# Optimization experiments

Measured on AMD Instinct MI355X. Metric: run time of the kernel, lower is better.

## Reference

```python
import jax, jax.numpy as jnp
import numpy as np

B, S, D = 4, 2048, 1024

def setup_inputs() -> dict:
    key = jax.random.key(0)
    k0, k1, k2, k3 = jax.random.split(key, 4)
    scale = 1.0 / np.sqrt(D)
    return {
        "x": jax.random.normal(k0, (B, S, D), dtype=jnp.float32),
        "Wq": jax.random.normal(k1, (D, D), dtype=jnp.float32) * scale,
        "Wk": jax.random.normal(k2, (D, D), dtype=jnp.float32) * scale,
        "Wv": jax.random.normal(k3, (D, D), dtype=jnp.float32) * scale,
    }

def reference(x, Wq, Wk, Wv):
    # x: [B,S,D]; Wq/Wk/Wv: [D_in, D_out] (equivalent to torch Linear weight transposed)
    q = jnp.einsum('bsd,de->bse', x, Wq)
    k = jnp.einsum('bsd,de->bse', x, Wk)
    v = jnp.einsum('bsd,de->bse', x, Wv)
    d_out = k.shape[-1]
    scores = jnp.einsum('bqe,bke->bqk', q, k)  # [B,S,S]
    S_ = scores.shape[-1]
    causal = jnp.tril(jnp.ones((S_, S_), dtype=bool))  # True = keep
    # masked_fill before scaling == after scaling (-inf invariant under positive scale)
    scores = jnp.where(causal, scores, -jnp.inf)
    attn = jax.nn.softmax(scores / jnp.sqrt(jnp.asarray(d_out, scores.dtype)), axis=-1)
    # dropout p=0.0 -> identity
    return jnp.einsum('bqk,bke->bqe', attn, v)
```

## Files before the change

### kernel.cpp

```cpp
#include <hip/hip_runtime.h>

#define B_  4
#define S_  2048
#define D_  1024
#define N_  (B_*S_)
#define SCALE 0.03125f
#define NEGINF (-3.0e38f)

typedef unsigned short u16;
typedef __attribute__((ext_vector_type(8))) short short8;
typedef __attribute__((ext_vector_type(4))) float floatx4;

__device__ __forceinline__ u16 f2bf(float f) {
    unsigned int u = __float_as_uint(f);
    u += 0x7FFFu + ((u >> 16) & 1u);
    return (u16)(u >> 16);
}
__device__ __forceinline__ float bf2f(u16 h) {
    return __uint_as_float((unsigned int)h << 16);
}

__device__ __forceinline__ void gl_lds16(const void* g, void* l) {
    __builtin_amdgcn_global_load_lds(
        (const __attribute__((address_space(1))) unsigned int*)g,
        (__attribute__((address_space(3))) unsigned int*)l, 16, 0, 0);
}

__device__ __forceinline__ int xcd_chunk(int bid, int nwg) {
    return (bid & 7) * (nwg >> 3) + (bid >> 3);
}

__global__ __launch_bounds__(256) void cast_fused(const float* __restrict__ x,
                                                  const float* __restrict__ Wq, const float* __restrict__ Wk,
                                                  const float* __restrict__ Wv,
                                                  u16* __restrict__ xb, u16* __restrict__ Wqb,
                                                  u16* __restrict__ Wkb, u16* __restrict__ Wvt) {
    __shared__ float t[32][33];
    const int blk = blockIdx.x;
    if (blk < 5120) {
        const float* src; u16* dst; size_t i;
        if (blk < 4096)      { src = x;  dst = xb;  i = (size_t)blk * 2048; }
        else if (blk < 4608) { src = Wq; dst = Wqb; i = (size_t)(blk - 4096) * 2048; }
        else                 { src = Wk; dst = Wkb; i = (size_t)(blk - 4608) * 2048; }
        i += (size_t)threadIdx.x * 8;
        float4 a = *(const float4*)&src[i];
        float4 b = *(const float4*)&src[i + 4];
        short8 o;
        o[0]=f2bf(a.x); o[1]=f2bf(a.y); o[2]=f2bf(a.z); o[3]=f2bf(a.w);
        o[4]=f2bf(b.x); o[5]=f2bf(b.y); o[6]=f2bf(b.z); o[7]=f2bf(b.w);
        *(short8*)&dst[i] = o;
    } else {
        const int tb = blk - 5120;
        const int c = threadIdx.x & 31, r0 = threadIdx.x >> 5;
        const int i0 = (tb >> 5) * 32, j0 = (tb & 31) * 32;
#pragma unroll
        for (int rr = 0; rr < 4; ++rr)
            t[r0 + rr * 8][c] = Wv[(size_t)(i0 + r0 + rr * 8) * D_ + j0 + c];
        __syncthreads();
#pragma unroll
        for (int rr = 0; rr < 4; ++rr)
            Wvt[(size_t)(j0 + r0 + rr * 8) * D_ + i0 + c] = f2bf(t[c][r0 + rr * 8]);
    }
}


__device__ __forceinline__ void mfma_nt_128(const u16* __restrict__ A, int lda,
                                            const u16* __restrict__ Bp, int ldb,
                                            int m0, int n0, int kext,
                                            u16* Sh, floatx4 acc[4][4])
{
    const int tid  = threadIdx.x;
    const int lane = tid & 63;
    const int lr   = lane & 15, quad = lane >> 4;
    const int wm   = ((tid >> 6) & 1) * 64, wn = (tid >> 7) * 64;
    const int nt   = kext >> 6;

    auto stage8 = [&](int t) {
#pragma unroll
        for (int h = 0; h < 8; ++h) {
            const int kk = h >> 2, mat = (h >> 1) & 1, half = h & 1;
            const int idx = tid * 8;
            const int row = half * 64 + (idx >> 5);
            const int s   = (idx & 31) >> 3;
            const int gk  = (t << 6) + kk * 32 + ((s ^ ((row >> 1) & 3)) << 3);
            u16* dst = Sh + (t & 1) * 16384 + mat * 8192 + kk * 4096 + half * 2048 + idx;
            const u16* src = mat ? &Bp[(size_t)(n0 + row) * ldb + gk]
                                 : &A [(size_t)(m0 + row) * lda + gk];
            gl_lds16(src, dst);
        }
    };

    stage8(0);
    for (int t = 0; t < nt; ++t) {
        asm volatile("s_waitcnt vmcnt(0)" ::: "memory");
        __builtin_amdgcn_s_barrier();
        if (t + 1 < nt) stage8(t + 1);
        const u16* buf = Sh + (t & 1) * 16384;
#pragma unroll
        for (int kk = 0; kk < 2; ++kk) {
            short8 af[4], bf[4];
#pragma unroll
            for (int i = 0; i < 4; ++i) {
                const int ar = wm + i * 16 + lr;
                af[i] = *(const short8*)&buf[kk * 4096 + ar * 32 + ((quad ^ ((ar >> 1) & 3)) << 3)];
                const int br = wn + i * 16 + lr;
                bf[i] = *(const short8*)&buf[8192 + kk * 4096 + br * 32 + ((quad ^ ((br >> 1) & 3)) << 3)];
            }
            __builtin_amdgcn_s_setprio(1);
#pragma unroll
            for (int i = 0; i < 4; ++i)
#pragma unroll
                for (int j = 0; j < 4; ++j)
                    acc[i][j] = __builtin_amdgcn_mfma_f32_16x16x32_bf16(af[i], bf[j], acc[i][j], 0, 0, 0);
            __builtin_amdgcn_s_setprio(0);
        }
    }
}

#define EPI_VARS                                              \
    const int lane = threadIdx.x & 63;                        \
    const int lr = lane & 15, quad = lane >> 4;               \
    const int wm = ((threadIdx.x >> 6) & 1) * 64, wn = (threadIdx.x >> 7) * 64;

__device__ __forceinline__ void mfma_nt_128w8(const u16* __restrict__ A, int lda,
                                              const u16* __restrict__ Bp, int ldb,
                                              int m0, int n0, int kext,
                                              u16* Sh, floatx4 acc[2][4])
{
    const int tid  = threadIdx.x;
    const int lane = tid & 63;
    const int lr   = lane & 15, quad = lane >> 4;
    const int wid  = tid >> 6;
    const int wm   = (wid >> 1) * 32;
    const int wn   = (wid & 1) * 64;
    const int nt   = kext >> 6;

    auto stage4 = [&](int t) {
#pragma unroll
        for (int h = 0; h < 4; ++h) {
            const int kk = h >> 1, mat = h & 1;
            const int idx = tid * 8;
            const int row = idx >> 5;
            const int s   = (idx & 31) >> 3;
            const int gk  = (t << 6) + kk * 32 + ((s ^ ((row >> 1) & 3)) << 3);
            u16* dst = Sh + (t & 1) * 16384 + mat * 8192 + kk * 4096 + idx;
            const u16* src = mat ? &Bp[(size_t)(n0 + row) * ldb + gk]
                                 : &A [(size_t)(m0 + row) * lda + gk];
            gl_lds16(src, dst);
        }
    };

    stage4(0);
    for (int t = 0; t < nt; ++t) {
        asm volatile("s_waitcnt vmcnt(0)" ::: "memory");
        __builtin_amdgcn_s_barrier();
        if (t + 1 < nt) stage4(t + 1);
        const u16* buf = Sh + (t & 1) * 16384;
#pragma unroll
        for (int kk = 0; kk < 2; ++kk) {
            short8 af[2], bf[4];
#pragma unroll
            for (int i = 0; i < 2; ++i) {
                const int ar = wm + i * 16 + lr;
                af[i] = *(const short8*)&buf[kk * 4096 + ar * 32 + ((quad ^ ((ar >> 1) & 3)) << 3)];
            }
#pragma unroll
            for (int j = 0; j < 4; ++j) {
                const int br = wn + j * 16 + lr;
                bf[j] = *(const short8*)&buf[8192 + kk * 4096 + br * 32 + ((quad ^ ((br >> 1) & 3)) << 3)];
            }
            __builtin_amdgcn_s_setprio(1);
#pragma unroll
            for (int i = 0; i < 2; ++i)
#pragma unroll
                for (int j = 0; j < 4; ++j)
                    acc[i][j] = __builtin_amdgcn_mfma_f32_16x16x32_bf16(af[i], bf[j], acc[i][j], 0, 0, 0);
            __builtin_amdgcn_s_setprio(0);
        }
    }
}

__device__ __forceinline__ void mfma_nt_256(const u16* __restrict__ A, int lda,
                                            const u16* __restrict__ Bp, int ldb,
                                            int m0, int n0, int kext,
                                            u16* Sh, floatx4 acc[8][4])
{
    const int tid  = threadIdx.x;
    const int lane = tid & 63;
    const int lr   = lane & 15, quad = lane >> 4;
    const int wr   = (tid >> 8) & 1, wc = (tid >> 6) & 3;
    const int nt   = kext >> 6;

    auto stage = [&](int t, int mat, int kk) {
#pragma unroll
        for (int pass = 0; pass < 2; ++pass) {
            const int idx = pass * 4096 + tid * 8;
            const int row = idx >> 5;
            const int s   = (idx & 31) >> 3;
            const int gk  = (t << 6) + kk * 32 + ((s ^ ((row >> 1) & 3)) << 3);
            u16* dst = Sh + (t & 1) * 32768 + mat * 16384 + kk * 8192 + idx;
            const u16* src = mat ? &Bp[(size_t)(n0 + row) * ldb + gk]
                                 : &A [(size_t)(m0 + row) * lda + gk];
            gl_lds16(src, dst);
        }
    };

    stage(0, 0, 0); stage(0, 1, 0); stage(0, 0, 1); stage(0, 1, 1);
    asm volatile("s_waitcnt vmcnt(4)" ::: "memory");
    __builtin_amdgcn_s_barrier();

    for (int t = 0; t < nt; ++t) {
        const u16* buf = Sh + (t & 1) * 32768;
        const bool pf = (t + 1 < nt);
        short8 af[4], bf[4];

#pragma unroll
        for (int kk = 0; kk < 2; ++kk) {
            const int kb = kk * 8192;

#pragma unroll
            for (int i = 0; i < 4; ++i) {
                const int ar = wr * 128 + i * 16 + lr;
                af[i] = *(const short8*)&buf[kb + ar * 32 + ((quad ^ ((ar >> 1) & 3)) << 3)];
            }
#pragma unroll
            for (int j = 0; j < 4; ++j) {
                const int br = wc * 64 + j * 16 + lr;
                bf[j] = *(const short8*)&buf[16384 + kb + br * 32 + ((quad ^ ((br >> 1) & 3)) << 3)];
            }
            if (pf) stage(t + 1, 0, kk);
            __builtin_amdgcn_s_barrier();
            asm volatile("s_waitcnt lgkmcnt(0)" ::: "memory");
            __builtin_amdgcn_s_setprio(1);
#pragma unroll
            for (int i = 0; i < 4; ++i)
#pragma unroll
                for (int j = 0; j < 4; ++j)
                    acc[i][j] = __builtin_amdgcn_mfma_f32_16x16x32_bf16(af[i], bf[j], acc[i][j], 0, 0, 0);
            __builtin_amdgcn_s_setprio(0);
            __builtin_amdgcn_s_barrier();

#pragma unroll
            for (int i = 0; i < 4; ++i) {
                const int ar = wr * 128 + 64 + i * 16 + lr;
                af[i] = *(const short8*)&buf[kb + ar * 32 + ((quad ^ ((ar >> 1) & 3)) << 3)];
            }
            if (pf) stage(t + 1, 1, kk);
            if (kk == 0) {
                if (pf) asm volatile("s_waitcnt vmcnt(4)" ::: "memory");
                else    asm volatile("s_waitcnt vmcnt(0)" ::: "memory");
            } else if (pf) {
                asm volatile("s_waitcnt vmcnt(4)" ::: "memory");
            }
            __builtin_amdgcn_s_barrier();
            asm volatile("s_waitcnt lgkmcnt(0)" ::: "memory");
            __builtin_amdgcn_s_setprio(1);
#pragma unroll
            for (int i = 0; i < 4; ++i)
#pragma unroll
                for (int j = 0; j < 4; ++j)
                    acc[4 + i][j] = __builtin_amdgcn_mfma_f32_16x16x32_bf16(af[i], bf[j], acc[4 + i][j], 0, 0, 0);
            __builtin_amdgcn_s_setprio(0);
            __builtin_amdgcn_s_barrier();
        }
    }
}

#define EPI256_VARS                                           \
    const int lane = threadIdx.x & 63;                        \
    const int lr = lane & 15, quad = lane >> 4;               \
    const int wr = (threadIdx.x >> 8) & 1, wc = (threadIdx.x >> 6) & 3;

__global__ __launch_bounds__(256) void mt_mfma(const u16* __restrict__ Wkb, const u16* __restrict__ Wqb,
                                               u16* __restrict__ Mt)
{
    __shared__ u16 Sh[32768];
    const int m0 = blockIdx.y * 128, n0 = blockIdx.x * 128;
    floatx4 acc[4][4];
#pragma unroll
    for (int i = 0; i < 4; ++i)
#pragma unroll
        for (int j = 0; j < 4; ++j) acc[i][j] = (floatx4){0.f, 0.f, 0.f, 0.f};
    mfma_nt_128(Wkb, D_, Wqb, D_, m0, n0, D_, Sh, acc);

    EPI_VARS
#pragma unroll
    for (int i = 0; i < 4; ++i)
#pragma unroll
        for (int j = 0; j < 4; ++j)
#pragma unroll
            for (int r = 0; r < 4; ++r)
                Mt[(size_t)(m0 + wm + i * 16 + quad * 4 + r) * D_ + n0 + wn + j * 16 + lr] = f2bf(acc[i][j][r]);
}

__global__ __launch_bounds__(512, 2) void yv_mfma(const u16* __restrict__ xb, const u16* __restrict__ Mt,
                                                  const u16* __restrict__ Wvt,
                                                  u16* __restrict__ Y, u16* __restrict__ Vt)
{
    __shared__ u16 Sh[65536];
    const int lid = xcd_chunk(blockIdx.x, 256);
    floatx4 acc[8][4];
#pragma unroll
    for (int i = 0; i < 8; ++i)
#pragma unroll
        for (int j = 0; j < 4; ++j) acc[i][j] = (floatx4){0.f, 0.f, 0.f, 0.f};

    if (lid < 128) {
        const int m0 = (lid >> 2) * 256, n0 = (lid & 3) * 256;
        mfma_nt_256(xb, D_, Mt, D_, m0, n0, D_, Sh, acc);
        EPI256_VARS
#pragma unroll
        for (int i = 0; i < 8; ++i)
#pragma unroll
            for (int j = 0; j < 4; ++j)
#pragma unroll
                for (int r = 0; r < 4; ++r)
                    Y[(size_t)(m0 + wr * 128 + i * 16 + quad * 4 + r) * D_ + n0 + wc * 64 + j * 16 + lr]
                        = f2bf(acc[i][j][r]);
    } else {
        const int v = lid - 128;
        const int b = v >> 5;
        const int mloc = ((v >> 2) & 7) * 256;
        const int n0 = (v & 3) * 256;
        const int m0 = b * S_ + mloc;
        u16* Vb = Vt + (size_t)b * D_ * S_;
        mfma_nt_256(xb, D_, Wvt, D_, m0, n0, D_, Sh, acc);
        EPI256_VARS
#pragma unroll
        for (int i = 0; i < 8; ++i)
#pragma unroll
            for (int j = 0; j < 4; ++j) {
                const int ee = n0 + wc * 64 + j * 16 + lr;
                const int s4 = mloc + wr * 128 + i * 16 + quad * 4;
                ushort4 o;
                o.x = f2bf(acc[i][j][0]); o.y = f2bf(acc[i][j][1]);
                o.z = f2bf(acc[i][j][2]); o.w = f2bf(acc[i][j][3]);
                *(ushort4*)&Vb[(size_t)ee * S_ + s4] = o;
            }
    }
}

__global__ __launch_bounds__(512, 2) void scores_mfma(const u16* __restrict__ Y, const u16* __restrict__ xb,
                                                      u16* __restrict__ Sc)
{
    __shared__ u16 Sh[65536];
    const int lid = xcd_chunk(blockIdx.x, 144);
    const int b = lid / 36;
    const int t = lid - b * 36;
    int qt = 0;
    while ((qt + 1) * (qt + 2) / 2 <= t) ++qt;
    const int kt = t - qt * (qt + 1) / 2;

    const u16* A  = Y  + (size_t)b * S_ * D_;
    const u16* Bp = xb + (size_t)b * S_ * D_;
    u16* Sb = Sc + (size_t)b * S_ * S_;
    const int m0 = qt * 256, n0 = kt * 256;
    floatx4 acc[8][4];
#pragma unroll
    for (int i = 0; i < 8; ++i)
#pragma unroll
        for (int j = 0; j < 4; ++j) acc[i][j] = (floatx4){0.f, 0.f, 0.f, 0.f};
    mfma_nt_256(A, D_, Bp, D_, m0, n0, D_, Sh, acc);

    EPI256_VARS
#pragma unroll
    for (int i = 0; i < 8; ++i)
#pragma unroll
        for (int r = 0; r < 4; ++r) {
            const int grow = m0 + wr * 128 + i * 16 + quad * 4 + r;
#pragma unroll
            for (int j = 0; j < 4; ++j) {
                const int gcol = n0 + wc * 64 + j * 16 + lr;
                const float v = (gcol <= grow) ? acc[i][j][r] * SCALE : NEGINF;
                Sb[(size_t)grow * S_ + gcol] = f2bf(v);
            }
        }
}

__global__ __launch_bounds__(256) void softmax_k(const u16* __restrict__ Sc, u16* __restrict__ P)
{
    const int row = blockIdx.x * 4 + (threadIdx.x >> 6);
    const int lane = threadIdx.x & 63;
    const int b = row >> 11, q = row & (S_ - 1);
    const int L = ((q >> 7) + 1) << 7;
    const u16* rp = Sc + ((size_t)b * S_ + q) * S_;
    u16* pp = P + ((size_t)b * S_ + q) * S_;

    float f[4][8];
    float lmax = -3.4e38f;
#pragma unroll
    for (int c = 0; c < 4; ++c) {
        const int i = c * 512 + lane * 8;
        if (i < L) {
            short8 v = *(const short8*)&rp[i];
#pragma unroll
            for (int k = 0; k < 8; ++k) { f[c][k] = bf2f((u16)v[k]); lmax = fmaxf(lmax, f[c][k]); }
        }
    }
#pragma unroll
    for (int off = 32; off; off >>= 1) lmax = fmaxf(lmax, __shfl_xor(lmax, off, 64));

    float lsum = 0.f;
#pragma unroll
    for (int c = 0; c < 4; ++c) {
        const int i = c * 512 + lane * 8;
        if (i < L) {
#pragma unroll
            for (int k = 0; k < 8; ++k) { f[c][k] = __expf(f[c][k] - lmax); lsum += f[c][k]; }
        }
    }
#pragma unroll
    for (int off = 32; off; off >>= 1) lsum += __shfl_xor(lsum, off, 64);
    const float inv = 1.0f / lsum;

#pragma unroll
    for (int c = 0; c < 4; ++c) {
        const int i = c * 512 + lane * 8;
        if (i < L) {
            short8 o;
#pragma unroll
            for (int k = 0; k < 8; ++k) o[k] = (short)f2bf(f[c][k] * inv);
            *(short8*)&pp[i] = o;
        }
    }
}

__device__ __forceinline__ void pv_epi(floatx4 acc[2][4], int b, int m0, int n0, float* __restrict__ O)
{
    const int lane = threadIdx.x & 63;
    const int lr = lane & 15, quad = lane >> 4;
    const int wid = threadIdx.x >> 6;
    const int wm = (wid >> 1) * 32, wn = (wid & 1) * 64;
#pragma unroll
    for (int i = 0; i < 2; ++i)
#pragma unroll
        for (int r = 0; r < 4; ++r) {
            const int grow = m0 + wm + i * 16 + quad * 4 + r;
#pragma unroll
            for (int j = 0; j < 4; ++j)
                O[((size_t)b * S_ + grow) * D_ + n0 + wn + j * 16 + lr] = acc[i][j][r];
        }
}

__global__ __launch_bounds__(512, 2) void pv_mfma(const u16* __restrict__ P, const u16* __restrict__ Vt,
                                                  float* __restrict__ O)
{
    __shared__ u16 Sh[32768];
    const int lid = xcd_chunk(blockIdx.x, 256);
    const int b  = lid >> 6;
    const int et = (lid >> 3) & 7;
    const int pr = lid & 7;
    const int n0 = et * 128;
    const u16* A  = P  + (size_t)b * S_ * S_;
    const u16* Bp = Vt + (size_t)b * D_ * S_;

    floatx4 acc[2][4];
    const int qtA = pr, qtB = 15 - pr;

#pragma unroll
    for (int i = 0; i < 2; ++i)
#pragma unroll
        for (int j = 0; j < 4; ++j) acc[i][j] = (floatx4){0.f, 0.f, 0.f, 0.f};
    mfma_nt_128w8(A, S_, Bp, S_, qtA * 128, n0, (qtA + 1) * 128, Sh, acc);
    pv_epi(acc, b, qtA * 128, n0, O);

#pragma unroll
    for (int i = 0; i < 2; ++i)
#pragma unroll
        for (int j = 0; j < 4; ++j) acc[i][j] = (floatx4){0.f, 0.f, 0.f, 0.f};
    mfma_nt_128w8(A, S_, Bp, S_, qtB * 128, n0, (qtB + 1) * 128, Sh, acc);
    pv_epi(acc, b, qtB * 128, n0, O);
}

extern "C" void kernel_launch(void* const* d_in, const int* in_sizes, int n_in,
                              void* d_out, int out_size, void* d_ws, size_t ws_size,
                              hipStream_t stream) {
    const float* x  = (const float*)d_in[0];
    const float* Wq = (const float*)d_in[1];
    const float* Wk = (const float*)d_in[2];
    const float* Wv = (const float*)d_in[3];
    float* out = (float*)d_out;
    char* w = (char*)d_ws;

    u16* xb  = (u16*)(w);
    u16* Wqb = (u16*)(w + 16777216);
    u16* Wkb = (u16*)(w + 18874368);
    u16* Wvt = (u16*)(w + 20971520);
    u16* Mt  = (u16*)(w + 23068672);
    u16* Y   = (u16*)(w + 25165824);
    u16* Vt  = (u16*)(w + 41943040);
    u16* Sc  = (u16*)(w + 58720256);
    u16* P   = (u16*)(w + 92274688);

    cast_fused <<<dim3(6144),   256, 0, stream>>>(x, Wq, Wk, Wv, xb, Wqb, Wkb, Wvt);
    mt_mfma    <<<dim3(8, 8),   256, 0, stream>>>(Wkb, Wqb, Mt);
    yv_mfma    <<<dim3(256),    512, 0, stream>>>(xb, Mt, Wvt, Y, Vt);
    scores_mfma<<<dim3(144),    512, 0, stream>>>(Y, xb, Sc);
    softmax_k  <<<dim3(N_/4),   256, 0, stream>>>(Sc, P);
    pv_mfma    <<<dim3(256),    512, 0, stream>>>(P, Vt, out);
}
```

Measured before the change: 209.9 us.

## Fuse softmax into scores epilogue and PV prologue via per-tile max/sum partials

```diff
diff --git a/kernel.cpp b/kernel.cpp
--- a/kernel.cpp
+++ b/kernel.cpp
@@ -122,10 +122,101 @@
     const int lr = lane & 15, quad = lane >> 4;               \
     const int wm = ((threadIdx.x >> 6) & 1) * 64, wn = (threadIdx.x >> 7) * 64;
 
-__device__ __forceinline__ void mfma_nt_128w8(const u16* __restrict__ A, int lda,
-                                              const u16* __restrict__ Bp, int ldb,
-                                              int m0, int n0, int kext,
-                                              u16* Sh, floatx4 acc[2][4])
+__device__ __forceinline__ void mfma_nt_256(const u16* __restrict__ A, int lda,
+                                            const u16* __restrict__ Bp, int ldb,
+                                            int m0, int n0, int kext,
+                                            u16* Sh, floatx4 acc[8][4])
+{
+    const int tid  = threadIdx.x;
+    const int lane = tid & 63;
+    const int lr   = lane & 15, quad = lane >> 4;
+    const int wr   = (tid >> 8) & 1, wc = (tid >> 6) & 3;
+    const int nt   = kext >> 6;
+
+    auto stage = [&](int t, int mat, int kk) {
+#pragma unroll
+        for (int pass = 0; pass < 2; ++pass) {
+            const int idx = pass * 4096 + tid * 8;
+            const int row = idx >> 5;
+            const int s   = (idx & 31) >> 3;
+            const int gk  = (t << 6) + kk * 32 + ((s ^ ((row >> 1) & 3)) << 3);
+            u16* dst = Sh + (t & 1) * 32768 + mat * 16384 + kk * 8192 + idx;
+            const u16* src = mat ? &Bp[(size_t)(n0 + row) * ldb + gk]
+                                 : &A [(size_t)(m0 + row) * lda + gk];
+            gl_lds16(src, dst);
+        }
+    };
+
+    stage(0, 0, 0); stage(0, 1, 0); stage(0, 0, 1); stage(0, 1, 1);
+    asm volatile("s_waitcnt vmcnt(4)" ::: "memory");
+    __builtin_amdgcn_s_barrier();
+
+    for (int t = 0; t < nt; ++t) {
+        const u16* buf = Sh + (t & 1) * 32768;
+        const bool pf = (t + 1 < nt);
+        short8 af[4], bf[4];
+
+#pragma unroll
+        for (int kk = 0; kk < 2; ++kk) {
+            const int kb = kk * 8192;
+
+#pragma unroll
+            for (int i = 0; i < 4; ++i) {
+                const int ar = wr * 128 + i * 16 + lr;
+                af[i] = *(const short8*)&buf[kb + ar * 32 + ((quad ^ ((ar >> 1) & 3)) << 3)];
+            }
+#pragma unroll
+            for (int j = 0; j < 4; ++j) {
+                const int br = wc * 64 + j * 16 + lr;
+                bf[j] = *(const short8*)&buf[16384 + kb + br * 32 + ((quad ^ ((br >> 1) & 3)) << 3)];
+            }
+            if (pf) stage(t + 1, 0, kk);
+            __builtin_amdgcn_s_barrier();
+            asm volatile("s_waitcnt lgkmcnt(0)" ::: "memory");
+            __builtin_amdgcn_s_setprio(1);
+#pragma unroll
+            for (int i = 0; i < 4; ++i)
+#pragma unroll
+                for (int j = 0; j < 4; ++j)
+                    acc[i][j] = __builtin_amdgcn_mfma_f32_16x16x32_bf16(af[i], bf[j], acc[i][j], 0, 0, 0);
+            __builtin_amdgcn_s_setprio(0);
+            __builtin_amdgcn_s_barrier();
+
+#pragma unroll
+            for (int i = 0; i < 4; ++i) {
+                const int ar = wr * 128 + 64 + i * 16 + lr;
+                af[i] = *(const short8*)&buf[kb + ar * 32 + ((quad ^ ((ar >> 1) & 3)) << 3)];
+            }
+            if (pf) stage(t + 1, 1, kk);
+            if (kk == 0) {
+                if (pf) asm volatile("s_waitcnt vmcnt(4)" ::: "memory");
+                else    asm volatile("s_waitcnt vmcnt(0)" ::: "memory");
+            } else if (pf) {
+                asm volatile("s_waitcnt vmcnt(4)" ::: "memory");
+            }
+            __builtin_amdgcn_s_barrier();
+            asm volatile("s_waitcnt lgkmcnt(0)" ::: "memory");
+            __builtin_amdgcn_s_setprio(1);
+#pragma unroll
+            for (int i = 0; i < 4; ++i)
+#pragma unroll
+                for (int j = 0; j < 4; ++j)
+                    acc[4 + i][j] = __builtin_amdgcn_mfma_f32_16x16x32_bf16(af[i], bf[j], acc[4 + i][j], 0, 0, 0);
+            __builtin_amdgcn_s_setprio(0);
+            __builtin_amdgcn_s_barrier();
+        }
+    }
+}
+
+#define EPI256_VARS                                           \
+    const int lane = threadIdx.x & 63;                        \
+    const int lr = lane & 15, quad = lane >> 4;               \
+    const int wr = (threadIdx.x >> 8) & 1, wc = (threadIdx.x >> 6) & 3;
+
+__device__ __forceinline__ void pv_loop(const u16* __restrict__ A, int lda,
+                                        const u16* __restrict__ Bp, int ldb,
+                                        int m0, int n0, int kext,
+                                        u16* Sh, float mA, float mB, floatx4 acc[2][4])
 {
     const int tid  = threadIdx.x;
     const int lane = tid & 63;
@@ -150,6 +241,14 @@
         }
     };
 
+    auto xf = [&](short8 a, float m) {
+        short8 o;
+#pragma unroll
+        for (int e = 0; e < 8; ++e)
+            o[e] = (short)f2bf(__expf(bf2f((u16)a[e]) - m));
+        return o;
+    };
+
     stage4(0);
     for (int t = 0; t < nt; ++t) {
         asm volatile("s_waitcnt vmcnt(0)" ::: "memory");
@@ -169,6 +268,8 @@
                 const int br = wn + j * 16 + lr;
                 bf[j] = *(const short8*)&buf[8192 + kk * 4096 + br * 32 + ((quad ^ ((br >> 1) & 3)) << 3)];
             }
+            af[0] = xf(af[0], mA);
+            af[1] = xf(af[1], mB);
             __builtin_amdgcn_s_setprio(1);
 #pragma unroll
             for (int i = 0; i < 2; ++i)
@@ -179,97 +280,6 @@
         }
     }
 }
-
-__device__ __forceinline__ void mfma_nt_256(const u16* __restrict__ A, int lda,
-                                            const u16* __restrict__ Bp, int ldb,
-                                            int m0, int n0, int kext,
-                                            u16* Sh, floatx4 acc[8][4])
-{
-    const int tid  = threadIdx.x;
-    const int lane = tid & 63;
-    const int lr   = lane & 15, quad = lane >> 4;
-    const int wr   = (tid >> 8) & 1, wc = (tid >> 6) & 3;
-    const int nt   = kext >> 6;
-
-    auto stage = [&](int t, int mat, int kk) {
-#pragma unroll
-        for (int pass = 0; pass < 2; ++pass) {
-            const int idx = pass * 4096 + tid * 8;
-            const int row = idx >> 5;
-            const int s   = (idx & 31) >> 3;
-            const int gk  = (t << 6) + kk * 32 + ((s ^ ((row >> 1) & 3)) << 3);
-            u16* dst = Sh + (t & 1) * 32768 + mat * 16384 + kk * 8192 + idx;
-            const u16* src = mat ? &Bp[(size_t)(n0 + row) * ldb + gk]
-                                 : &A [(size_t)(m0 + row) * lda + gk];
-            gl_lds16(src, dst);
-        }
-    };
-
-    stage(0, 0, 0); stage(0, 1, 0); stage(0, 0, 1); stage(0, 1, 1);
-    asm volatile("s_waitcnt vmcnt(4)" ::: "memory");
-    __builtin_amdgcn_s_barrier();
-
-    for (int t = 0; t < nt; ++t) {
-        const u16* buf = Sh + (t & 1) * 32768;
-        const bool pf = (t + 1 < nt);
-        short8 af[4], bf[4];
-
-#pragma unroll
-        for (int kk = 0; kk < 2; ++kk) {
-            const int kb = kk * 8192;
-
-#pragma unroll
-            for (int i = 0; i < 4; ++i) {
-                const int ar = wr * 128 + i * 16 + lr;
-                af[i] = *(const short8*)&buf[kb + ar * 32 + ((quad ^ ((ar >> 1) & 3)) << 3)];
-            }
-#pragma unroll
-            for (int j = 0; j < 4; ++j) {
-                const int br = wc * 64 + j * 16 + lr;
-                bf[j] = *(const short8*)&buf[16384 + kb + br * 32 + ((quad ^ ((br >> 1) & 3)) << 3)];
-            }
-            if (pf) stage(t + 1, 0, kk);
-            __builtin_amdgcn_s_barrier();
-            asm volatile("s_waitcnt lgkmcnt(0)" ::: "memory");
-            __builtin_amdgcn_s_setprio(1);
-#pragma unroll
-            for (int i = 0; i < 4; ++i)
-#pragma unroll
-                for (int j = 0; j < 4; ++j)
-                    acc[i][j] = __builtin_amdgcn_mfma_f32_16x16x32_bf16(af[i], bf[j], acc[i][j], 0, 0, 0);
-            __builtin_amdgcn_s_setprio(0);
-            __builtin_amdgcn_s_barrier();
-
-#pragma unroll
-            for (int i = 0; i < 4; ++i) {
-                const int ar = wr * 128 + 64 + i * 16 + lr;
-                af[i] = *(const short8*)&buf[kb + ar * 32 + ((quad ^ ((ar >> 1) & 3)) << 3)];
-            }
-            if (pf) stage(t + 1, 1, kk);
-            if (kk == 0) {
-                if (pf) asm volatile("s_waitcnt vmcnt(4)" ::: "memory");
-                else    asm volatile("s_waitcnt vmcnt(0)" ::: "memory");
-            } else if (pf) {
-                asm volatile("s_waitcnt vmcnt(4)" ::: "memory");
-            }
-            __builtin_amdgcn_s_barrier();
-            asm volatile("s_waitcnt lgkmcnt(0)" ::: "memory");
-            __builtin_amdgcn_s_setprio(1);
-#pragma unroll
-            for (int i = 0; i < 4; ++i)
-#pragma unroll
-                for (int j = 0; j < 4; ++j)
-                    acc[4 + i][j] = __builtin_amdgcn_mfma_f32_16x16x32_bf16(af[i], bf[j], acc[4 + i][j], 0, 0, 0);
-            __builtin_amdgcn_s_setprio(0);
-            __builtin_amdgcn_s_barrier();
-        }
-    }
-}
-
-#define EPI256_VARS                                           \
-    const int lane = threadIdx.x & 63;                        \
-    const int lr = lane & 15, quad = lane >> 4;               \
-    const int wr = (threadIdx.x >> 8) & 1, wc = (threadIdx.x >> 6) & 3;
 
 __global__ __launch_bounds__(256) void mt_mfma(const u16* __restrict__ Wkb, const u16* __restrict__ Wqb,
                                                u16* __restrict__ Mt)
@@ -341,19 +351,20 @@
 }
 
 __global__ __launch_bounds__(512, 2) void scores_mfma(const u16* __restrict__ Y, const u16* __restrict__ xb,
-                                                      u16* __restrict__ Sc)
+                                                      u16* __restrict__ Sc,
+                                                      float* __restrict__ Pm, float* __restrict__ Ps)
 {
     __shared__ u16 Sh[65536];
     const int lid = xcd_chunk(blockIdx.x, 144);
-    const int b = lid / 36;
-    const int t = lid - b * 36;
+    const int bb = lid / 36;
+    const int t = lid - bb * 36;
     int qt = 0;
     while ((qt + 1) * (qt + 2) / 2 <= t) ++qt;
     const int kt = t - qt * (qt + 1) / 2;
 
-    const u16* A  = Y  + (size_t)b * S_ * D_;
-    const u16* Bp = xb + (size_t)b * S_ * D_;
-    u16* Sb = Sc + (size_t)b * S_ * S_;
+    const u16* A  = Y  + (size_t)bb * S_ * D_;
+    const u16* Bp = xb + (size_t)bb * S_ * D_;
+    u16* Sb = Sc + (size_t)bb * S_ * S_;
     const int m0 = qt * 256, n0 = kt * 256;
     floatx4 acc[8][4];
 #pragma unroll
@@ -363,113 +374,116 @@
     mfma_nt_256(A, D_, Bp, D_, m0, n0, D_, Sh, acc);
 
     EPI256_VARS
+    const int tid = threadIdx.x;
+    const int kt256 = n0 >> 8;
+    float* redM = (float*)Sh;
+    float* redS = redM + 1024;
+
 #pragma unroll
     for (int i = 0; i < 8; ++i)
 #pragma unroll
         for (int r = 0; r < 4; ++r) {
-            const int grow = m0 + wr * 128 + i * 16 + quad * 4 + r;
+            const int rl   = wr * 128 + i * 16 + quad * 4 + r;
+            const int grow = m0 + rl;
+            float vm = NEGINF;
 #pragma unroll
             for (int j = 0; j < 4; ++j) {
                 const int gcol = n0 + wc * 64 + j * 16 + lr;
                 const float v = (gcol <= grow) ? acc[i][j][r] * SCALE : NEGINF;
                 Sb[(size_t)grow * S_ + gcol] = f2bf(v);
-            }
-        }
-}
-
-__global__ __launch_bounds__(256) void softmax_k(const u16* __restrict__ Sc, u16* __restrict__ P)
-{
-    const int row = blockIdx.x * 4 + (threadIdx.x >> 6);
-    const int lane = threadIdx.x & 63;
-    const int b = row >> 11, q = row & (S_ - 1);
-    const int L = ((q >> 7) + 1) << 7;
-    const u16* rp = Sc + ((size_t)b * S_ + q) * S_;
-    u16* pp = P + ((size_t)b * S_ + q) * S_;
-
-    float f[4][8];
-    float lmax = -3.4e38f;
-#pragma unroll
-    for (int c = 0; c < 4; ++c) {
-        const int i = c * 512 + lane * 8;
-        if (i < L) {
-            short8 v = *(const short8*)&rp[i];
-#pragma unroll
-            for (int k = 0; k < 8; ++k) { f[c][k] = bf2f((u16)v[k]); lmax = fmaxf(lmax, f[c][k]); }
-        }
-    }
-#pragma unroll
-    for (int off = 32; off; off >>= 1) lmax = fmaxf(lmax, __shfl_xor(lmax, off, 64));
-
-    float lsum = 0.f;
-#pragma unroll
-    for (int c = 0; c < 4; ++c) {
-        const int i = c * 512 + lane * 8;
-        if (i < L) {
-#pragma unroll
-            for (int k = 0; k < 8; ++k) { f[c][k] = __expf(f[c][k] - lmax); lsum += f[c][k]; }
-        }
-    }
-#pragma unroll
-    for (int off = 32; off; off >>= 1) lsum += __shfl_xor(lsum, off, 64);
-    const float inv = 1.0f / lsum;
-
-#pragma unroll
-    for (int c = 0; c < 4; ++c) {
-        const int i = c * 512 + lane * 8;
-        if (i < L) {
-            short8 o;
-#pragma unroll
-            for (int k = 0; k < 8; ++k) o[k] = (short)f2bf(f[c][k] * inv);
-            *(short8*)&pp[i] = o;
-        }
-    }
-}
-
-__device__ __forceinline__ void pv_epi(floatx4 acc[2][4], int b, int m0, int n0, float* __restrict__ O)
-{
-    const int lane = threadIdx.x & 63;
+                vm = fmaxf(vm, v);
+            }
+#pragma unroll
+            for (int off = 1; off < 16; off <<= 1) vm = fmaxf(vm, __shfl_xor(vm, off, 64));
+            if (lr == 0) redM[wc * 256 + rl] = vm;
+        }
+    __syncthreads();
+    if (tid < 256) {
+        const float m4 = fmaxf(fmaxf(redM[tid], redM[256 + tid]),
+                               fmaxf(redM[512 + tid], redM[768 + tid]));
+        redM[tid] = m4;
+        Pm[((size_t)bb * 2048 + m0 + tid) * 8 + kt256] = m4;
+    }
+    __syncthreads();
+#pragma unroll
+    for (int i = 0; i < 8; ++i)
+#pragma unroll
+        for (int r = 0; r < 4; ++r) {
+            const int rl   = wr * 128 + i * 16 + quad * 4 + r;
+            const int grow = m0 + rl;
+            const float m = redM[rl];
+            float s = 0.f;
+#pragma unroll
+            for (int j = 0; j < 4; ++j) {
+                const int gcol = n0 + wc * 64 + j * 16 + lr;
+                if (gcol <= grow) s += __expf(acc[i][j][r] * SCALE - m);
+            }
+#pragma unroll
+            for (int off = 1; off < 16; off <<= 1) s += __shfl_xor(s, off, 64);
+            if (lr == 0) redS[wc * 256 + rl] = s;
+        }
+    __syncthreads();
+    if (tid < 256)
+        Ps[((size_t)bb * 2048 + m0 + tid) * 8 + kt256] =
+            redS[tid] + redS[256 + tid] + redS[512 + tid] + redS[768 + tid];
+}
+
+__global__ __launch_bounds__(512, 2) void pv_mfma(const u16* __restrict__ Sc, const u16* __restrict__ Vt,
+                                                  const float* __restrict__ Pm, const float* __restrict__ Ps,
+                                                  float* __restrict__ O)
+{
+    __shared__ u16 Sh[32768];
+    __shared__ float Mtab[128], Itab[128];
+    const int lid = xcd_chunk(blockIdx.x, 512);
+    const int s  = lid >> 5;
+    const int be = lid & 31;
+    const int b  = be >> 3, et = be & 7;
+    const int qt = (s & 1) ? 15 - (s >> 1) : (s >> 1);
+    const int m0 = qt * 128, n0 = et * 128;
+    const int kext = (qt + 1) * 128;
+    const u16* A  = Sc + (size_t)b * S_ * S_;
+    const u16* Bp = Vt + (size_t)b * D_ * S_;
+
+    const int tid = threadIdx.x;
+    if (tid < 128) {
+        const int g = m0 + tid;
+        const int nkt = (g >> 8) + 1;
+        const float* pm = Pm + ((size_t)b * 2048 + g) * 8;
+        const float* ps = Ps + ((size_t)b * 2048 + g) * 8;
+        float M = NEGINF;
+        for (int k = 0; k < nkt; ++k) M = fmaxf(M, pm[k]);
+        float Ssum = 0.f;
+        for (int k = 0; k < nkt; ++k) Ssum += ps[k] * __expf(pm[k] - M);
+        Mtab[tid] = M;
+        Itab[tid] = 1.0f / Ssum;
+    }
+    __syncthreads();
+
+    const int lane = tid & 63;
     const int lr = lane & 15, quad = lane >> 4;
-    const int wid = threadIdx.x >> 6;
+    const int wid = tid >> 6;
     const int wm = (wid >> 1) * 32, wn = (wid & 1) * 64;
+    const float mA = Mtab[wm + lr];
+    const float mB = Mtab[wm + 16 + lr];
+
+    floatx4 acc[2][4];
 #pragma unroll
     for (int i = 0; i < 2; ++i)
 #pragma unroll
+        for (int j = 0; j < 4; ++j) acc[i][j] = (floatx4){0.f, 0.f, 0.f, 0.f};
+    pv_loop(A, S_, Bp, S_, m0, n0, kext, Sh, mA, mB, acc);
+
+#pragma unroll
+    for (int i = 0; i < 2; ++i)
+#pragma unroll
         for (int r = 0; r < 4; ++r) {
-            const int grow = m0 + wm + i * 16 + quad * 4 + r;
+            const int rl = wm + i * 16 + quad * 4 + r;
+            const float inv = Itab[rl];
+            const int grow = m0 + rl;
 #pragma unroll
             for (int j = 0; j < 4; ++j)
-                O[((size_t)b * S_ + grow) * D_ + n0 + wn + j * 16 + lr] = acc[i][j][r];
-        }
-}
-
-__global__ __launch_bounds__(512, 2) void pv_mfma(const u16* __restrict__ P, const u16* __restrict__ Vt,
-                                                  float* __restrict__ O)
-{
-    __shared__ u16 Sh[32768];
-    const int lid = xcd_chunk(blockIdx.x, 256);
-    const int b  = lid >> 6;
-    const int et = (lid >> 3) & 7;
-    const int pr = lid & 7;
-    const int n0 = et * 128;
-    const u16* A  = P  + (size_t)b * S_ * S_;
-    const u16* Bp = Vt + (size_t)b * D_ * S_;
-
-    floatx4 acc[2][4];
-    const int qtA = pr, qtB = 15 - pr;
-
-#pragma unroll
-    for (int i = 0; i < 2; ++i)
-#pragma unroll
-        for (int j = 0; j < 4; ++j) acc[i][j] = (floatx4){0.f, 0.f, 0.f, 0.f};
-    mfma_nt_128w8(A, S_, Bp, S_, qtA * 128, n0, (qtA + 1) * 128, Sh, acc);
-    pv_epi(acc, b, qtA * 128, n0, O);
-
-#pragma unroll
-    for (int i = 0; i < 2; ++i)
-#pragma unroll
-        for (int j = 0; j < 4; ++j) acc[i][j] = (floatx4){0.f, 0.f, 0.f, 0.f};
-    mfma_nt_128w8(A, S_, Bp, S_, qtB * 128, n0, (qtB + 1) * 128, Sh, acc);
-    pv_epi(acc, b, qtB * 128, n0, O);
+                O[((size_t)b * S_ + grow) * D_ + n0 + wn + j * 16 + lr] = acc[i][j][r] * inv;
+        }
 }
 
 extern "C" void kernel_launch(void* const* d_in, const int* in_sizes, int n_in,
@@ -490,12 +504,12 @@
     u16* Y   = (u16*)(w + 25165824);
     u16* Vt  = (u16*)(w + 41943040);
     u16* Sc  = (u16*)(w + 58720256);
-    u16* P   = (u16*)(w + 92274688);
+    float* Pm = (float*)(w + 92274688);
+    float* Ps = (float*)(w + 92536832);
 
     cast_fused <<<dim3(6144),   256, 0, stream>>>(x, Wq, Wk, Wv, xb, Wqb, Wkb, Wvt);
     mt_mfma    <<<dim3(8, 8),   256, 0, stream>>>(Wkb, Wqb, Mt);
     yv_mfma    <<<dim3(256),    512, 0, stream>>>(xb, Mt, Wvt, Y, Vt);
-    scores_mfma<<<dim3(144),    512, 0, stream>>>(Y, xb, Sc);
-    softmax_k  <<<dim3(N_/4),   256, 0, stream>>>(Sc, P);
-    pv_mfma    <<<dim3(256),    512, 0, stream>>>(P, Vt, out);
-}
+    scores_mfma<<<dim3(144),    512, 0, stream>>>(Y, xb, Sc, Pm, Ps);
+    pv_mfma    <<<dim3(512),    512, 0, stream>>>(Sc, Vt, Pm, Ps, out);
+}
```

New measurement: 247.6 us. +18.0%, slower.

## Shrink scores tiles to 128 and split PV pairs into separate blocks

Applied to the files above, without the earlier changes.

```diff
diff --git a/kernel.cpp b/kernel.cpp
--- a/kernel.cpp
+++ b/kernel.cpp
@@ -180,6 +180,12 @@
     }
 }
 
+#define EPIW8_VARS                                            \
+    const int lane = threadIdx.x & 63;                        \
+    const int lr = lane & 15, quad = lane >> 4;               \
+    const int wid = threadIdx.x >> 6;                         \
+    const int wm = (wid >> 1) * 32, wn = (wid & 1) * 64;
+
 __device__ __forceinline__ void mfma_nt_256(const u16* __restrict__ A, int lda,
                                             const u16* __restrict__ Bp, int ldb,
                                             int m0, int n0, int kext,
@@ -343,34 +349,35 @@
 __global__ __launch_bounds__(512, 2) void scores_mfma(const u16* __restrict__ Y, const u16* __restrict__ xb,
                                                       u16* __restrict__ Sc)
 {
-    __shared__ u16 Sh[65536];
-    const int lid = xcd_chunk(blockIdx.x, 144);
-    const int b = lid / 36;
-    const int t = lid - b * 36;
-    int qt = 0;
+    __shared__ u16 Sh[32768];
+    const int lid = xcd_chunk(blockIdx.x, 544);
+    const int b = lid / 136;
+    const int t = lid - b * 136;
+    int qt = (int)((sqrtf(8.0f * t + 1.0f) - 1.0f) * 0.5f);
     while ((qt + 1) * (qt + 2) / 2 <= t) ++qt;
+    while (qt * (qt + 1) / 2 > t) --qt;
     const int kt = t - qt * (qt + 1) / 2;
 
     const u16* A  = Y  + (size_t)b * S_ * D_;
     const u16* Bp = xb + (size_t)b * S_ * D_;
     u16* Sb = Sc + (size_t)b * S_ * S_;
-    const int m0 = qt * 256, n0 = kt * 256;
-    floatx4 acc[8][4];
-#pragma unroll
-    for (int i = 0; i < 8; ++i)
+    const int m0 = qt * 128, n0 = kt * 128;
+    floatx4 acc[2][4];
+#pragma unroll
+    for (int i = 0; i < 2; ++i)
 #pragma unroll
         for (int j = 0; j < 4; ++j) acc[i][j] = (floatx4){0.f, 0.f, 0.f, 0.f};
-    mfma_nt_256(A, D_, Bp, D_, m0, n0, D_, Sh, acc);
-
-    EPI256_VARS
-#pragma unroll
-    for (int i = 0; i < 8; ++i)
+    mfma_nt_128w8(A, D_, Bp, D_, m0, n0, D_, Sh, acc);
+
+    EPIW8_VARS
+#pragma unroll
+    for (int i = 0; i < 2; ++i)
 #pragma unroll
         for (int r = 0; r < 4; ++r) {
-            const int grow = m0 + wr * 128 + i * 16 + quad * 4 + r;
+            const int grow = m0 + wm + i * 16 + quad * 4 + r;
 #pragma unroll
             for (int j = 0; j < 4; ++j) {
-                const int gcol = n0 + wc * 64 + j * 16 + lr;
+                const int gcol = n0 + wn + j * 16 + lr;
                 const float v = (gcol <= grow) ? acc[i][j][r] * SCALE : NEGINF;
                 Sb[(size_t)grow * S_ + gcol] = f2bf(v);
             }
@@ -425,12 +432,28 @@
     }
 }
 
-__device__ __forceinline__ void pv_epi(floatx4 acc[2][4], int b, int m0, int n0, float* __restrict__ O)
-{
-    const int lane = threadIdx.x & 63;
-    const int lr = lane & 15, quad = lane >> 4;
-    const int wid = threadIdx.x >> 6;
-    const int wm = (wid >> 1) * 32, wn = (wid & 1) * 64;
+__global__ __launch_bounds__(512, 2) void pv_mfma(const u16* __restrict__ P, const u16* __restrict__ Vt,
+                                                  float* __restrict__ O)
+{
+    __shared__ u16 Sh[32768];
+    const int lid = xcd_chunk(blockIdx.x, 512);
+    const int s  = lid >> 5;
+    const int be = lid & 31;
+    const int b  = be >> 3, et = be & 7;
+    const int qt = (s & 1) ? 15 - (s >> 1) : (s >> 1);
+    const int m0 = qt * 128, n0 = et * 128;
+    const int kext = (qt + 1) * 128;
+    const u16* A  = P  + (size_t)b * S_ * S_;
+    const u16* Bp = Vt + (size_t)b * D_ * S_;
+
+    floatx4 acc[2][4];
+#pragma unroll
+    for (int i = 0; i < 2; ++i)
+#pragma unroll
+        for (int j = 0; j < 4; ++j) acc[i][j] = (floatx4){0.f, 0.f, 0.f, 0.f};
+    mfma_nt_128w8(A, S_, Bp, S_, m0, n0, kext, Sh, acc);
+
+    EPIW8_VARS
 #pragma unroll
     for (int i = 0; i < 2; ++i)
 #pragma unroll
@@ -440,36 +463,6 @@
             for (int j = 0; j < 4; ++j)
                 O[((size_t)b * S_ + grow) * D_ + n0 + wn + j * 16 + lr] = acc[i][j][r];
         }
-}
-
-__global__ __launch_bounds__(512, 2) void pv_mfma(const u16* __restrict__ P, const u16* __restrict__ Vt,
-                                                  float* __restrict__ O)
-{
-    __shared__ u16 Sh[32768];
-    const int lid = xcd_chunk(blockIdx.x, 256);
-    const int b  = lid >> 6;
-    const int et = (lid >> 3) & 7;
-    const int pr = lid & 7;
-    const int n0 = et * 128;
-    const u16* A  = P  + (size_t)b * S_ * S_;
-    const u16* Bp = Vt + (size_t)b * D_ * S_;
-
-    floatx4 acc[2][4];
-    const int qtA = pr, qtB = 15 - pr;
-
-#pragma unroll
-    for (int i = 0; i < 2; ++i)
-#pragma unroll
-        for (int j = 0; j < 4; ++j) acc[i][j] = (floatx4){0.f, 0.f, 0.f, 0.f};
-    mfma_nt_128w8(A, S_, Bp, S_, qtA * 128, n0, (qtA + 1) * 128, Sh, acc);
-    pv_epi(acc, b, qtA * 128, n0, O);
-
-#pragma unroll
-    for (int i = 0; i < 2; ++i)
-#pragma unroll
-        for (int j = 0; j < 4; ++j) acc[i][j] = (floatx4){0.f, 0.f, 0.f, 0.f};
-    mfma_nt_128w8(A, S_, Bp, S_, qtB * 128, n0, (qtB + 1) * 128, Sh, acc);
-    pv_epi(acc, b, qtB * 128, n0, O);
 }
 
 extern "C" void kernel_launch(void* const* d_in, const int* in_sizes, int n_in,
@@ -495,7 +488,7 @@
     cast_fused <<<dim3(6144),   256, 0, stream>>>(x, Wq, Wk, Wv, xb, Wqb, Wkb, Wvt);
     mt_mfma    <<<dim3(8, 8),   256, 0, stream>>>(Wkb, Wqb, Mt);
     yv_mfma    <<<dim3(256),    512, 0, stream>>>(xb, Mt, Wvt, Y, Vt);
-    scores_mfma<<<dim3(144),    512, 0, stream>>>(Y, xb, Sc);
+    scores_mfma<<<dim3(544),    512, 0, stream>>>(Y, xb, Sc);
     softmax_k  <<<dim3(N_/4),   256, 0, stream>>>(Sc, P);
-    pv_mfma    <<<dim3(256),    512, 0, stream>>>(P, Vt, out);
-}
+    pv_mfma    <<<dim3(512),    512, 0, stream>>>(P, Vt, out);
+}
```

Measured after the change: 211.2 us. No clear change (+0.6%).
